# Optimization experiments

Measured on AMD Instinct MI355X. Metric: run time of the kernel, lower is better.

## Reference

```python
import jax, jax.numpy as jnp
import numpy as np

B, T, D = 32, 1024, 384
T_OUT = 4096  # static padded output length (= target_len for every batch element)


def setup_inputs() -> dict:
    key = jax.random.key(0)
    k1, k2 = jax.random.split(key)
    x = jax.random.normal(k1, (B, T, D), dtype=jnp.float32)
    durations = jax.random.randint(k2, (B, T), 0, 8, dtype=jnp.int32)
    # constant target length -> torch pads/truncates every row to T_OUT,
    # and max over batch is T_OUT, so output is [B, T_OUT, D].
    target_len = jnp.full((B,), T_OUT, dtype=jnp.int32)
    return {"x": x, "durations": durations, "target_len": target_len}


def reference(x, durations, target_len):
    # x: [B, T, D]; durations: [B, T] int; target_len: [B] int.
    # Ragged repeat-expansion expressed as cumulative-duration searchsorted + gather.
    Bx, Tx, Dx = x.shape
    dur = jnp.maximum(durations, 0)
    ends = jnp.cumsum(dur, axis=1)              # [B, T] exclusive-end frame index per token
    total = ends[:, -1]                          # [B] total expanded length per batch row
    pos = jnp.arange(T_OUT, dtype=ends.dtype)    # [T_OUT] output frame positions
    # token index owning each output frame: number of ends <= pos
    idx = jax.vmap(lambda e: jnp.searchsorted(e, pos, side="right"))(ends)  # [B, T_OUT]
    idx = jnp.clip(idx, 0, Tx - 1)
    out = jnp.take_along_axis(x, idx[..., None], axis=1)  # [B, T_OUT, D]
    # frames past min(total_expansion, target_len) are zero padding (truncate + pad semantics)
    limit = jnp.minimum(total, target_len.astype(total.dtype))  # [B]
    valid = pos[None, :] < limit[:, None]                        # [B, T_OUT]
    return jnp.where(valid[..., None], out, jnp.zeros((), x.dtype))
```

## Files before the change

kernel.cpp:

```cpp
#include <hip/hip_runtime.h>


#define BB 32
#define TT 1024
#define TOUT 4096
#define D4 96
#define N4 (TOUT * D4)
#define EPB 3072
#define ROWS_PB 32
#define KPT 12
#define NBLK (BB * (N4 / EPB))
#define NXCD 8
#define PER_XCD (NBLK / NXCD)

typedef float v4f __attribute__((ext_vector_type(4)));

__global__ __launch_bounds__(256) void lr_fused(
    const int4* __restrict__ dur4,
    const int* __restrict__ target_len,
    const v4f* __restrict__ x,
    v4f* __restrict__ out)
{
    __shared__ int s_ends[TT];
    __shared__ int s_wsum[4];
    __shared__ int s_trow[ROWS_PB];

    const int flat = blockIdx.x;
    const int newid = (flat & (NXCD - 1)) * PER_XCD + (flat >> 3);
    const int b = newid >> 7;
    const int chunk = newid & 127;

    const int tid = threadIdx.x;
    const int lane = tid & 63;
    const int wave = tid >> 6;
    const int base0 = chunk * EPB;
    const int p0 = chunk * ROWS_PB;

    const int tl = target_len[b];

    int4 d = dur4[b * 256 + tid];
    const int d0 = d.x > 0 ? d.x : 0;
    const int d1 = d.y > 0 ? d.y : 0;
    const int d2 = d.z > 0 ? d.z : 0;
    const int d3 = d.w > 0 ? d.w : 0;
    const int e0 = d0, e1 = e0 + d1, e2 = e1 + d2, e3 = e2 + d3;

    int v = e3;
    #pragma unroll
    for (int off = 1; off < 64; off <<= 1) {
        int u = __shfl_up(v, off, 64);
        if (lane >= off) v += u;
    }
    if (lane == 63) s_wsum[wave] = v;
    __syncthreads();

    int wbase = 0;
    #pragma unroll
    for (int w = 0; w < 3; ++w) wbase += (w < wave) ? s_wsum[w] : 0;
    const int total = s_wsum[0] + s_wsum[1] + s_wsum[2] + s_wsum[3];
    const int lim = total < tl ? total : tl;

    const int base = wbase + v - e3;
    ((int4*)s_ends)[tid] = make_int4(base + e0, base + e1, base + e2, base + e3);
    __syncthreads();

    if (tid < ROWS_PB) {
        const int p = p0 + tid;
        int lo = 0;
        #pragma unroll
        for (int s = 512; s > 0; s >>= 1) {
            lo += (s_ends[lo + s - 1] <= p) ? s : 0;
        }
        s_trow[tid] = lo;
    }
    __syncthreads();

    const v4f* __restrict__ x_b = x + b * TT * D4;
    v4f* __restrict__ out_b = out + b * N4;

    int pp[KPT], cc[KPT], tt[KPT];
    v4f vv[KPT];
    #pragma unroll
    for (int k = 0; k < KPT; ++k) {
        const int i = base0 + k * 256 + tid;
        const int p = i / D4;
        pp[k] = p;
        cc[k] = i - p * D4;
        tt[k] = s_trow[p - p0];
    }
    #pragma unroll
    for (int k = 0; k < KPT; ++k) {
        vv[k] = x_b[tt[k] * D4 + cc[k]];
    }
    #pragma unroll
    for (int k = 0; k < KPT; ++k) {
        if (pp[k] >= lim) vv[k] = (v4f)(0.f);
        __builtin_nontemporal_store(vv[k], out_b + base0 + k * 256 + tid);
    }
}

extern "C" void kernel_launch(void* const* d_in, const int* in_sizes, int n_in,
                              void* d_out, int out_size, void* d_ws, size_t ws_size,
                              hipStream_t stream) {
    const float* x        = (const float*)d_in[0];
    const int* durations  = (const int*)d_in[1];
    const int* target_len = (const int*)d_in[2];
    float* out            = (float*)d_out;

    lr_fused<<<dim3(NBLK), 256, 0, stream>>>((const int4*)durations, target_len,
                                             (const v4f*)x, (v4f*)out);
}
```

Measured before the change: 239.8 us.

## Stage contiguous source rows into LDS via global_load_lds before expansion

When a block's 32 output frames map to at most 30 distinct source tokens, the kernel bulk-copies that contiguous row span of x into LDS using direct global-to-LDS loads, then builds the output from LDS. This replaces repeated, scattered per-frame global gathers with one coalesced read of each needed row. The cost is about 47KB of extra shared memory per block, which lowers occupancy, plus an extra barrier. Blocks whose span exceeds 30 rows fall back to the old direct-gather path. The row index is also clamped to stay in bounds.

Measured after the change: 239.8 us. About the same (-0.0%).

```diff
diff --git a/kernel.cpp b/kernel.cpp
--- a/kernel.cpp
+++ b/kernel.cpp
@@ -9,9 +9,12 @@
 #define EPB 3072
 #define ROWS_PB 32
 #define KPT 12
-#define NBLK (BB * (N4 / EPB))
+#define NBLK 4096
 #define NXCD 8
 #define PER_XCD (NBLK / NXCD)
+#define SROWS 30
+#define ROWB (D4 * 16)
+#define SBYTES (SROWS * ROWB)
 
 typedef float v4f __attribute__((ext_vector_type(4)));
 
@@ -24,6 +27,7 @@
     __shared__ int s_ends[TT];
     __shared__ int s_wsum[4];
     __shared__ int s_trow[ROWS_PB];
+    __shared__ v4f s_x[(SBYTES + 1024) / 16];
 
     const int flat = blockIdx.x;
     const int newid = (flat & (NXCD - 1)) * PER_XCD + (flat >> 3);
@@ -71,31 +75,61 @@
         for (int s = 512; s > 0; s >>= 1) {
             lo += (s_ends[lo + s - 1] <= p) ? s : 0;
         }
-        s_trow[tid] = lo;
+        s_trow[tid] = lo < (TT - 1) ? lo : (TT - 1);
     }
     __syncthreads();
 
     const v4f* __restrict__ x_b = x + b * TT * D4;
     v4f* __restrict__ out_b = out + b * N4;
 
-    int pp[KPT], cc[KPT], tt[KPT];
-    v4f vv[KPT];
-    #pragma unroll
-    for (int k = 0; k < KPT; ++k) {
-        const int i = base0 + k * 256 + tid;
-        const int p = i / D4;
-        pp[k] = p;
-        cc[k] = i - p * D4;
-        tt[k] = s_trow[p - p0];
-    }
-    #pragma unroll
-    for (int k = 0; k < KPT; ++k) {
-        vv[k] = x_b[tt[k] * D4 + cc[k]];
-    }
-    #pragma unroll
-    for (int k = 0; k < KPT; ++k) {
-        if (pp[k] >= lim) vv[k] = (v4f)(0.f);
-        __builtin_nontemporal_store(vv[k], out_b + base0 + k * 256 + tid);
+    const int t_lo = s_trow[0];
+    const int t_hi = s_trow[ROWS_PB - 1];
+    const int nrows = t_hi - t_lo + 1;
+
+    if (nrows <= SROWS) {
+        const int nbytes = nrows * ROWB;
+        const char* gsrc = (const char*)(x_b + t_lo * D4);
+        const char* gend = (const char*)(x_b + TT * D4) - 16;
+        for (int off = wave * 1024; off < nbytes; off += 4096) {
+            const char* g = gsrc + off + (lane << 4);
+            if (g > gend) g = gend;
+            __builtin_amdgcn_global_load_lds(
+                (const __attribute__((address_space(1))) void*)g,
+                (__attribute__((address_space(3))) void*)((char*)s_x + off),
+                16, 0, 0);
+        }
+        __syncthreads();
+
+        #pragma unroll
+        for (int k = 0; k < KPT; ++k) {
+            const int i = base0 + k * 256 + tid;
+            const int p = i / D4;
+            const int c = i - p * D4;
+            const int t = s_trow[p - p0];
+            v4f val = s_x[(t - t_lo) * D4 + c];
+            if (p >= lim) val = (v4f)(0.f);
+            __builtin_nontemporal_store(val, out_b + i);
+        }
+    } else {
+        int pp[KPT], cc[KPT], tt[KPT];
+        v4f vv[KPT];
+        #pragma unroll
+        for (int k = 0; k < KPT; ++k) {
+            const int i = base0 + k * 256 + tid;
+            const int p = i / D4;
+            pp[k] = p;
+            cc[k] = i - p * D4;
+            tt[k] = s_trow[p - p0];
+        }
+        #pragma unroll
+        for (int k = 0; k < KPT; ++k) {
+            vv[k] = x_b[tt[k] * D4 + cc[k]];
+        }
+        #pragma unroll
+        for (int k = 0; k < KPT; ++k) {
+            if (pp[k] >= lim) vv[k] = (v4f)(0.f);
+            __builtin_nontemporal_store(vv[k], out_b + base0 + k * 256 + tid);
+        }
     }
 }
 
```
